# Kernel tuning notes

Measured on AMD Instinct MI355X. Metric: run time of the kernel, lower is better.

Reference implementation:

```python
import jax, jax.numpy as jnp
import numpy as np

N = 32768
E = 262144
OUT = 512
H = 8
DH = OUT // H


def setup_inputs() -> dict:
    key = jax.random.key(0)
    ks = jax.random.split(key, 12)
    s = 0.02
    return {
        "h": jax.random.normal(ks[0], (N, 512), dtype=jnp.float32),
        "row": jax.random.randint(ks[1], (E,), 0, N, dtype=jnp.int32),
        "col": jax.random.randint(ks[2], (E,), 0, N, dtype=jnp.int32),
        "W_in": jax.random.normal(ks[3], (512, OUT), dtype=jnp.float32) * s,
        "b_in": jnp.zeros((OUT,), dtype=jnp.float32),
        "W_q": jax.random.normal(ks[4], (OUT, OUT), dtype=jnp.float32) * s,
        "b_q": jnp.zeros((OUT,), dtype=jnp.float32),
        "W_k": jax.random.normal(ks[5], (OUT, OUT), dtype=jnp.float32) * s,
        "b_k": jnp.zeros((OUT,), dtype=jnp.float32),
        "W_v": jax.random.normal(ks[6], (OUT, OUT), dtype=jnp.float32) * s,
        "b_v": jnp.zeros((OUT,), dtype=jnp.float32),
    }


def reference(h, row, col, W_in, b_in, W_q, b_q, W_k, b_k, W_v, b_v):
    scaling = DH ** -0.5
    x = h @ W_in + b_in                                   # [N, OUT]
    q = ((x @ W_q + b_q) * scaling).reshape(N, H, DH)     # [N, H, DH]
    k = (x @ W_k + b_k).reshape(N, H, DH)
    v = (x @ W_v + b_v).reshape(N, H, DH)

    # bsddmm: per-edge, per-head attention logits only at adjacency nonzeros
    logits = jnp.einsum("ehd,ehd->eh", q[row], k[col])    # [E, H]

    # sparse row-wise softmax over each node's incident edges
    m = jax.ops.segment_max(logits, row, num_segments=N)  # [N, H]
    ex = jnp.exp(logits - m[row])                         # [E, H]
    denom = jax.ops.segment_sum(ex, row, num_segments=N)  # [N, H]
    attn = ex / denom[row]                                # [E, H]

    # bspmm: aggregate v over neighbors with sparse attention weights
    out = jax.ops.segment_sum(attn[:, :, None] * v[col], row, num_segments=N)  # [N, H, DH]
    return out
```

## Files before the change

kernel.cpp:

```cpp
#include <hip/hip_runtime.h>

#define NN 32768
#define EE 262144
#define DM 512
#define NQKV 1536
#define NHEAD 8
#define DHEAD 64

typedef unsigned short u16;
typedef unsigned int u32;
typedef __attribute__((ext_vector_type(8))) short bf16x8;
typedef __attribute__((ext_vector_type(4))) float f32x4;
typedef __attribute__((ext_vector_type(8))) u16 u16x8;
typedef __attribute__((ext_vector_type(4))) u32 u32x4;

__device__ __forceinline__ float bf2f(u16 u) {
  union { u32 i; float f; } x; x.i = ((u32)u) << 16; return x.f;
}
__device__ __forceinline__ float bflo(u32 p) {
  union { u32 i; float f; } x; x.i = p << 16; return x.f;
}
__device__ __forceinline__ float bfhi(u32 p) {
  union { u32 i; float f; } x; x.i = p & 0xFFFF0000u; return x.f;
}
__device__ __forceinline__ u16 f2bf(float f) {
  union { float f; u32 i; } x; x.f = f;
  u32 r = x.i + 0x7FFFu + ((x.i >> 16) & 1u);
  return (u16)(r >> 16);
}

__device__ __forceinline__ void load_lds16(const u16* g, u16* l) {
  __builtin_amdgcn_global_load_lds(
      (const __attribute__((address_space(1))) char*)(const void*)g,
      (__attribute__((address_space(3))) char*)(void*)l, 16, 0, 0);
}

__global__ void tcast_w(const float* __restrict__ Wq, const float* __restrict__ Wk,
                        const float* __restrict__ Wv, u16* __restrict__ At) {
  const int z = blockIdx.z;
  const float* W = (z == 0) ? Wq : (z == 1) ? Wk : Wv;
  const float scale = (z == 0) ? 0.125f : 1.0f;
  const int m0 = blockIdx.x * 64;
  const int j0 = blockIdx.y * 64;
  __shared__ float t[64][65];
  const int tx = threadIdx.x & 63, ty = threadIdx.x >> 6;
#pragma unroll
  for (int i = 0; i < 16; ++i) {
    const int r = ty * 16 + i;
    t[r][tx] = W[(size_t)(m0 + r) * 512 + (j0 + tx)];
  }
  __syncthreads();
#pragma unroll
  for (int i = 0; i < 16; ++i) {
    const int j = ty * 16 + i;
    At[(size_t)(z * 512 + j0 + j) * 512 + (m0 + tx)] = f2bf(t[tx][j] * scale);
  }
}

__global__ void cast_win(const float* __restrict__ Win, u16* __restrict__ Winb) {
  const int i = (blockIdx.x * 256 + threadIdx.x) * 8;
  float4 a = *(const float4*)&Win[i];
  float4 b = *(const float4*)&Win[i + 4];
  u16x8 o = { f2bf(a.x), f2bf(a.y), f2bf(a.z), f2bf(a.w),
              f2bf(b.x), f2bf(b.y), f2bf(b.z), f2bf(b.w) };
  *(u16x8*)&Winb[i] = o;
}

__global__ void make_bias(const float* __restrict__ bin,
                          const float* __restrict__ Wq, const float* __restrict__ bq,
                          const float* __restrict__ Wk, const float* __restrict__ bk,
                          const float* __restrict__ Wv, const float* __restrict__ bv,
                          float* __restrict__ bias) {
  const int j = blockIdx.x * 256 + threadIdx.x;
  if (j >= 1536) return;
  const float* Wsel; const float* bsel; int jj; float scale = 1.0f;
  if (j < 512)       { Wsel = Wq; bsel = bq; jj = j;        scale = 0.125f; }
  else if (j < 1024) { Wsel = Wk; bsel = bk; jj = j - 512;  }
  else               { Wsel = Wv; bsel = bv; jj = j - 1024; }
  float s = 0.f;
  for (int m = 0; m < 512; ++m) s = fmaf(bin[m], Wsel[m * 512 + jj], s);
  bias[j] = (s + bsel[jj]) * scale;
}

__global__ void cast_h(const float* __restrict__ h, u16* __restrict__ hb) {
  const int i = (blockIdx.x * 256 + threadIdx.x) * 8;
  float4 a = *(const float4*)&h[i];
  float4 b = *(const float4*)&h[i + 4];
  u16x8 o = { f2bf(a.x), f2bf(a.y), f2bf(a.z), f2bf(a.w),
              f2bf(b.x), f2bf(b.y), f2bf(b.z), f2bf(b.w) };
  *(u16x8*)&hb[i] = o;
}

__global__ void count_deg(const int* __restrict__ row, int* __restrict__ deg) {
  const int e = blockIdx.x * 256 + threadIdx.x;
  atomicAdd(&deg[row[e]], 1);
}

__global__ void scan_deg(const int* __restrict__ deg, int* __restrict__ row_ptr,
                         int* __restrict__ cursor) {
  __shared__ int sums[1024];
  const int t = threadIdx.x;
  const int base = t * 32;
  int loc[32];
  int s = 0;
#pragma unroll
  for (int i = 0; i < 32; ++i) { loc[i] = s; s += deg[base + i]; }
  sums[t] = s;
  __syncthreads();
  for (int off = 1; off < 1024; off <<= 1) {
    int v = (t >= off) ? sums[t - off] : 0;
    __syncthreads();
    sums[t] += v;
    __syncthreads();
  }
  const int excl = sums[t] - s;
#pragma unroll
  for (int i = 0; i < 32; ++i) {
    const int val = excl + loc[i];
    row_ptr[base + i] = val;
    cursor[base + i] = val;
  }
  if (t == 1023) row_ptr[NN] = sums[1023];
}

__global__ void fill_csr(const int* __restrict__ row, const int* __restrict__ col,
                         int* __restrict__ cursor, int* __restrict__ dst) {
  const int e = blockIdx.x * 256 + threadIdx.x;
  const int r = row[e];
  const int p = atomicAdd(&cursor[r], 1);
  dst[p] = col[e];
}

__global__ __launch_bounds__(256, 2) void gemm_wt(
    const u16* __restrict__ A,
    const u16* __restrict__ B,
    u16* __restrict__ C) {
  __shared__ u16 As[128 * 32];
  __shared__ u16 Bs[128 * 32];
  const int tid = threadIdx.x;
  const int lane = tid & 63;
  const int wave = tid >> 6;
  const int quad = lane >> 4;
  const int l16 = lane & 15;
  const int m0 = blockIdx.y * 128;
  const int n0 = blockIdx.x * 128;
  const int wm = (wave >> 1) * 64;
  const int wn = (wave & 1) * 64;

  const int c0 = tid, c1 = tid + 256;
  const int r0 = c0 >> 2, ko0 = (c0 & 3) * 8;
  const int r1 = c1 >> 2, ko1 = (c1 & 3) * 8;
  const u16* Ag0 = A + (size_t)(m0 + r0) * DM + ko0;
  const u16* Ag1 = A + (size_t)(m0 + r1) * DM + ko1;
  const u16* Bg0 = B + (size_t)(n0 + r0) * DM + ko0;
  const u16* Bg1 = B + (size_t)(n0 + r1) * DM + ko1;
  u16* Al0 = &As[c0 * 8]; u16* Al1 = &As[c1 * 8];
  u16* Bl0 = &Bs[c0 * 8]; u16* Bl1 = &Bs[c1 * 8];

  f32x4 acc[4][4];
#pragma unroll
  for (int i = 0; i < 4; ++i)
#pragma unroll
    for (int j = 0; j < 4; ++j) acc[i][j] = (f32x4){0.f, 0.f, 0.f, 0.f};

  for (int kt = 0; kt < DM; kt += 32) {
    load_lds16(Ag0 + kt, Al0);
    load_lds16(Bg0 + kt, Bl0);
    load_lds16(Ag1 + kt, Al1);
    load_lds16(Bg1 + kt, Bl1);
    __syncthreads();
    bf16x8 a[4], b[4];
#pragma unroll
    for (int i = 0; i < 4; ++i) {
      a[i] = *(const bf16x8*)&As[(wm + i * 16 + l16) * 32 + quad * 8];
      b[i] = *(const bf16x8*)&Bs[(wn + i * 16 + l16) * 32 + quad * 8];
    }
#pragma unroll
    for (int mi = 0; mi < 4; ++mi)
#pragma unroll
      for (int ni = 0; ni < 4; ++ni)
        acc[mi][ni] = __builtin_amdgcn_mfma_f32_16x16x32_bf16(a[mi], b[ni], acc[mi][ni], 0, 0, 0);
    __syncthreads();
  }

#pragma unroll
  for (int ni = 0; ni < 4; ++ni) {
    const int coln = n0 + wn + ni * 16 + l16;
#pragma unroll
    for (int mi = 0; mi < 4; ++mi) {
#pragma unroll
      for (int r = 0; r < 4; ++r) {
        const int rowm = m0 + wm + mi * 16 + quad * 4 + r;
        C[(size_t)rowm * 512 + coln] = f2bf(acc[mi][ni][r]);
      }
    }
  }
}

__global__ __launch_bounds__(256, 2) void gemm_qkv(
    const u16* __restrict__ A,
    const u16* __restrict__ B,
    const float* __restrict__ bias,
    u16* __restrict__ Cq,
    u16* __restrict__ Ckv) {
  __shared__ u16 As[128 * 32];
  __shared__ u16 Bs[128 * 32];
  const int tid = threadIdx.x;
  const int lane = tid & 63;
  const int wave = tid >> 6;
  const int quad = lane >> 4;
  const int l16 = lane & 15;
  const int m0 = blockIdx.y * 128;
  const int n0 = blockIdx.x * 128;
  const int wm = (wave >> 1) * 64;
  const int wn = (wave & 1) * 64;

  const int c0 = tid, c1 = tid + 256;
  const int r0 = c0 >> 2, ko0 = (c0 & 3) * 8;
  const int r1 = c1 >> 2, ko1 = (c1 & 3) * 8;
  const u16* Ag0 = A + (size_t)(m0 + r0) * DM + ko0;
  const u16* Ag1 = A + (size_t)(m0 + r1) * DM + ko1;
  const u16* Bg0 = B + (size_t)(n0 + r0) * DM + ko0;
  const u16* Bg1 = B + (size_t)(n0 + r1) * DM + ko1;
  u16* Al0 = &As[c0 * 8]; u16* Al1 = &As[c1 * 8];
  u16* Bl0 = &Bs[c0 * 8]; u16* Bl1 = &Bs[c1 * 8];

  f32x4 acc[4][4];
#pragma unroll
  for (int i = 0; i < 4; ++i)
#pragma unroll
    for (int j = 0; j < 4; ++j) acc[i][j] = (f32x4){0.f, 0.f, 0.f, 0.f};

  for (int kt = 0; kt < DM; kt += 32) {
    load_lds16(Ag0 + kt, Al0);
    load_lds16(Bg0 + kt, Bl0);
    load_lds16(Ag1 + kt, Al1);
    load_lds16(Bg1 + kt, Bl1);
    __syncthreads();
    bf16x8 a[4], b[4];
#pragma unroll
    for (int i = 0; i < 4; ++i) {
      a[i] = *(const bf16x8*)&As[(wm + i * 16 + l16) * 32 + quad * 8];
      b[i] = *(const bf16x8*)&Bs[(wn + i * 16 + l16) * 32 + quad * 8];
    }
#pragma unroll
    for (int mi = 0; mi < 4; ++mi)
#pragma unroll
      for (int ni = 0; ni < 4; ++ni)
        acc[mi][ni] = __builtin_amdgcn_mfma_f32_16x16x32_bf16(a[mi], b[ni], acc[mi][ni], 0, 0, 0);
    __syncthreads();
  }

#pragma unroll
  for (int ni = 0; ni < 4; ++ni) {
    const int coln = n0 + wn + ni * 16 + l16;
    const float bv = bias[coln];
    const int isq = coln < 512;
    const int sel = coln >= 1024;
    const int d = coln - 512 - (sel << 9);
#pragma unroll
    for (int mi = 0; mi < 4; ++mi) {
#pragma unroll
      for (int r = 0; r < 4; ++r) {
        const int rowm = m0 + wm + mi * 16 + quad * 4 + r;
        const u16 val = f2bf(acc[mi][ni][r] + bv);
        if (isq) Cq[(size_t)rowm * 512 + coln] = val;
        else     Ckv[(size_t)rowm * 1024 + d * 2 + sel] = val;
      }
    }
  }
}

__global__ __launch_bounds__(256) void attn_agg(
    const u16* __restrict__ q, const u32* __restrict__ kv,
    const int* __restrict__ row_ptr, const int* __restrict__ dst,
    float* __restrict__ out) {
  const int gt = blockIdx.x * 256 + threadIdx.x;
  const int node = gt >> 6;
  const int lane = gt & 63;
  const u16x8 qr = *(const u16x8*)&q[(size_t)node * 512 + lane * 8];
  float qf[8];
#pragma unroll
  for (int j = 0; j < 8; ++j) qf[j] = bf2f(qr[j]);

  const int beg = row_ptr[node];
  const int end = row_ptr[node + 1];
  float acc[8] = {0.f,0.f,0.f,0.f,0.f,0.f,0.f,0.f};
  float denom = 0.f;

  for (int e = beg; e < end; e += 4) {
    u32 p[4][8];
    int idx[4];
#pragma unroll
    for (int jj = 0; jj < 4; ++jj) {
      const int ee = min(e + jj, end - 1);
      idx[jj] = dst[ee];
    }
#pragma unroll
    for (int jj = 0; jj < 4; ++jj) {
      const u32* pp = kv + ((size_t)idx[jj] << 9) + lane * 8;
      *(u32x4*)&p[jj][0] = *(const u32x4*)pp;
      *(u32x4*)&p[jj][4] = *(const u32x4*)(pp + 4);
    }
#pragma unroll
    for (int jj = 0; jj < 4; ++jj) {
      float s = 0.f;
#pragma unroll
      for (int j = 0; j < 8; ++j) s = fmaf(qf[j], bflo(p[jj][j]), s);
      s += __shfl_xor(s, 1, 64);
      s += __shfl_xor(s, 2, 64);
      s += __shfl_xor(s, 4, 64);
      const float ex = (e + jj < end) ? __expf(s) : 0.f;
      denom += ex;
#pragma unroll
      for (int j = 0; j < 8; ++j) acc[j] = fmaf(ex, bfhi(p[jj][j]), acc[j]);
    }
  }

  const float inv = (end > beg) ? (1.0f / denom) : 0.f;
  float4 o0 = { acc[0] * inv, acc[1] * inv, acc[2] * inv, acc[3] * inv };
  float4 o1 = { acc[4] * inv, acc[5] * inv, acc[6] * inv, acc[7] * inv };
  float* op = &out[(size_t)node * 512 + lane * 8];
  *(float4*)op = o0;
  *(float4*)(op + 4) = o1;
}

extern "C" void kernel_launch(void* const* d_in, const int* in_sizes, int n_in,
                              void* d_out, int out_size, void* d_ws, size_t ws_size,
                              hipStream_t stream) {
  const float* h   = (const float*)d_in[0];
  const int*   row = (const int*)d_in[1];
  const int*   col = (const int*)d_in[2];
  const float* Win = (const float*)d_in[3];
  const float* bin = (const float*)d_in[4];
  const float* Wq  = (const float*)d_in[5];
  const float* bq  = (const float*)d_in[6];
  const float* Wk  = (const float*)d_in[7];
  const float* bk  = (const float*)d_in[8];
  const float* Wv  = (const float*)d_in[9];
  const float* bv  = (const float*)d_in[10];
  float* out = (float*)d_out;

  char* ws = (char*)d_ws;
  u16*   qbuf    = (u16*)(ws + 0);
  u16*   kvbuf   = (u16*)(ws + 33554432);
  u16*   hb      = (u16*)(ws + 100663296);
  u16*   Wt      = (u16*)(ws + 134217728);
  float* bias    = (float*)(ws + 135790592);
  int*   deg     = (int*)(ws + 135796736);
  int*   row_ptr = (int*)(ws + 135927808);
  int*   cursor  = (int*)(ws + 136058888);
  int*   dst     = (int*)(ws + 136189960);
  u16*   At      = (u16*)(ws + 0);
  u16*   Winb    = (u16*)(ws + 1572864);

  (void)hipMemsetAsync(deg, 0, NN * sizeof(int), stream);
  hipLaunchKernelGGL(tcast_w,   dim3(8, 8, 3), dim3(256), 0, stream, Wq, Wk, Wv, At);
  hipLaunchKernelGGL(cast_win,  dim3((512 * 512 / 8) / 256), dim3(256), 0, stream, Win, Winb);
  hipLaunchKernelGGL(make_bias, dim3(6), dim3(256), 0, stream, bin, Wq, bq, Wk, bk, Wv, bv, bias);
  hipLaunchKernelGGL(cast_h,    dim3((NN * DM / 8) / 256), dim3(256), 0, stream, h, hb);
  hipLaunchKernelGGL(count_deg, dim3(EE / 256), dim3(256), 0, stream, row, deg);
  hipLaunchKernelGGL(scan_deg,  dim3(1), dim3(1024), 0, stream, deg, row_ptr, cursor);
  hipLaunchKernelGGL(fill_csr,  dim3(EE / 256), dim3(256), 0, stream, row, col, cursor, dst);
  hipLaunchKernelGGL(gemm_wt,   dim3(512 / 128, 1536 / 128), dim3(256), 0, stream, At, Winb, Wt);
  hipLaunchKernelGGL(gemm_qkv,  dim3(NQKV / 128, NN / 128), dim3(256), 0, stream, hb, Wt, bias, qbuf, kvbuf);
  hipLaunchKernelGGL(attn_agg,  dim3((NN * 64) / 256), dim3(256), 0, stream,
                     qbuf, (const u32*)kvbuf, row_ptr, dst, out);
}
```

Measured before the change: 394.7 us.

## Swizzle GEMM LDS tiles and interleave K/V via weight row permutation

Applies an XOR swizzle to the LDS tile layout in both GEMMs so the MFMA fragment reads spread across banks instead of conflicting. It also permutes the fused weight and bias rows so K and V columns come out interleaved directly from the GEMM. That lets gemm_qkv write one contiguous [N,1536] output instead of scattered conditional stores, and attn_agg reads the interleaved KV from that unified buffer. The cost is a wider row stride (1536) for the gathered KV reads.

Result: faster. 379.1 us (-4.0%).

```diff
diff --git a/kernel.cpp b/kernel.cpp
--- a/kernel.cpp
+++ b/kernel.cpp
@@ -34,6 +34,11 @@
       (const __attribute__((address_space(1))) char*)(const void*)g,
       (__attribute__((address_space(3))) char*)(void*)l, 16, 0, 0);
 }
+
+__device__ __forceinline__ int swz(int r, int s) {
+  return s ^ (r & 3) ^ ((r >> 2) & 1);
+}
+
 
 __global__ void tcast_w(const float* __restrict__ Wq, const float* __restrict__ Wk,
                         const float* __restrict__ Wv, u16* __restrict__ At) {
@@ -52,8 +57,9 @@
   __syncthreads();
 #pragma unroll
   for (int i = 0; i < 16; ++i) {
-    const int j = ty * 16 + i;
-    At[(size_t)(z * 512 + j0 + j) * 512 + (m0 + tx)] = f2bf(t[tx][j] * scale);
+    const int j = j0 + ty * 16 + i;
+    const int pr = (z == 0) ? j : (512 + 2 * j + (z - 1));
+    At[(size_t)pr * 512 + (m0 + tx)] = f2bf(t[tx][ty * 16 + i] * scale);
   }
 }
 
@@ -73,13 +79,13 @@
                           float* __restrict__ bias) {
   const int j = blockIdx.x * 256 + threadIdx.x;
   if (j >= 1536) return;
-  const float* Wsel; const float* bsel; int jj; float scale = 1.0f;
-  if (j < 512)       { Wsel = Wq; bsel = bq; jj = j;        scale = 0.125f; }
-  else if (j < 1024) { Wsel = Wk; bsel = bk; jj = j - 512;  }
-  else               { Wsel = Wv; bsel = bv; jj = j - 1024; }
+  const float* Wsel; const float* bsel; int jj; float scale = 1.0f; int pos;
+  if (j < 512)       { Wsel = Wq; bsel = bq; jj = j;        scale = 0.125f; pos = j; }
+  else if (j < 1024) { Wsel = Wk; bsel = bk; jj = j - 512;  pos = 512 + 2 * jj; }
+  else               { Wsel = Wv; bsel = bv; jj = j - 1024; pos = 513 + 2 * jj; }
   float s = 0.f;
   for (int m = 0; m < 512; ++m) s = fmaf(bin[m], Wsel[m * 512 + jj], s);
-  bias[j] = (s + bsel[jj]) * scale;
+  bias[pos] = (s + bsel[jj]) * scale;
 }
 
 __global__ void cast_h(const float* __restrict__ h, u16* __restrict__ hb) {
@@ -148,8 +154,8 @@
   const int wn = (wave & 1) * 64;
 
   const int c0 = tid, c1 = tid + 256;
-  const int r0 = c0 >> 2, ko0 = (c0 & 3) * 8;
-  const int r1 = c1 >> 2, ko1 = (c1 & 3) * 8;
+  const int r0 = c0 >> 2, ko0 = swz(r0, c0 & 3) * 8;
+  const int r1 = c1 >> 2, ko1 = swz(r1, c1 & 3) * 8;
   const u16* Ag0 = A + (size_t)(m0 + r0) * DM + ko0;
   const u16* Ag1 = A + (size_t)(m0 + r1) * DM + ko1;
   const u16* Bg0 = B + (size_t)(n0 + r0) * DM + ko0;
@@ -172,8 +178,10 @@
     bf16x8 a[4], b[4];
 #pragma unroll
     for (int i = 0; i < 4; ++i) {
-      a[i] = *(const bf16x8*)&As[(wm + i * 16 + l16) * 32 + quad * 8];
-      b[i] = *(const bf16x8*)&Bs[(wn + i * 16 + l16) * 32 + quad * 8];
+      const int ra = wm + i * 16 + l16;
+      const int rb = wn + i * 16 + l16;
+      a[i] = *(const bf16x8*)&As[ra * 32 + swz(ra, quad) * 8];
+      b[i] = *(const bf16x8*)&Bs[rb * 32 + swz(rb, quad) * 8];
     }
 #pragma unroll
     for (int mi = 0; mi < 4; ++mi)
@@ -201,8 +209,7 @@
     const u16* __restrict__ A,
     const u16* __restrict__ B,
     const float* __restrict__ bias,
-    u16* __restrict__ Cq,
-    u16* __restrict__ Ckv) {
+    u16* __restrict__ C) {
   __shared__ u16 As[128 * 32];
   __shared__ u16 Bs[128 * 32];
   const int tid = threadIdx.x;
@@ -216,8 +223,8 @@
   const int wn = (wave & 1) * 64;
 
   const int c0 = tid, c1 = tid + 256;
-  const int r0 = c0 >> 2, ko0 = (c0 & 3) * 8;
-  const int r1 = c1 >> 2, ko1 = (c1 & 3) * 8;
+  const int r0 = c0 >> 2, ko0 = swz(r0, c0 & 3) * 8;
+  const int r1 = c1 >> 2, ko1 = swz(r1, c1 & 3) * 8;
   const u16* Ag0 = A + (size_t)(m0 + r0) * DM + ko0;
   const u16* Ag1 = A + (size_t)(m0 + r1) * DM + ko1;
   const u16* Bg0 = B + (size_t)(n0 + r0) * DM + ko0;
@@ -240,8 +247,10 @@
     bf16x8 a[4], b[4];
 #pragma unroll
     for (int i = 0; i < 4; ++i) {
-      a[i] = *(const bf16x8*)&As[(wm + i * 16 + l16) * 32 + quad * 8];
-      b[i] = *(const bf16x8*)&Bs[(wn + i * 16 + l16) * 32 + quad * 8];
+      const int ra = wm + i * 16 + l16;
+      const int rb = wn + i * 16 + l16;
+      a[i] = *(const bf16x8*)&As[ra * 32 + swz(ra, quad) * 8];
+      b[i] = *(const bf16x8*)&Bs[rb * 32 + swz(rb, quad) * 8];
     }
 #pragma unroll
     for (int mi = 0; mi < 4; ++mi)
@@ -255,30 +264,25 @@
   for (int ni = 0; ni < 4; ++ni) {
     const int coln = n0 + wn + ni * 16 + l16;
     const float bv = bias[coln];
-    const int isq = coln < 512;
-    const int sel = coln >= 1024;
-    const int d = coln - 512 - (sel << 9);
 #pragma unroll
     for (int mi = 0; mi < 4; ++mi) {
 #pragma unroll
       for (int r = 0; r < 4; ++r) {
         const int rowm = m0 + wm + mi * 16 + quad * 4 + r;
-        const u16 val = f2bf(acc[mi][ni][r] + bv);
-        if (isq) Cq[(size_t)rowm * 512 + coln] = val;
-        else     Ckv[(size_t)rowm * 1024 + d * 2 + sel] = val;
+        C[(size_t)rowm * NQKV + coln] = f2bf(acc[mi][ni][r] + bv);
       }
     }
   }
 }
 
 __global__ __launch_bounds__(256) void attn_agg(
-    const u16* __restrict__ q, const u32* __restrict__ kv,
+    const u16* __restrict__ qkv16, const u32* __restrict__ qkv32,
     const int* __restrict__ row_ptr, const int* __restrict__ dst,
     float* __restrict__ out) {
   const int gt = blockIdx.x * 256 + threadIdx.x;
   const int node = gt >> 6;
   const int lane = gt & 63;
-  const u16x8 qr = *(const u16x8*)&q[(size_t)node * 512 + lane * 8];
+  const u16x8 qr = *(const u16x8*)&qkv16[(size_t)node * NQKV + lane * 8];
   float qf[8];
 #pragma unroll
   for (int j = 0; j < 8; ++j) qf[j] = bf2f(qr[j]);
@@ -298,7 +302,7 @@
     }
 #pragma unroll
     for (int jj = 0; jj < 4; ++jj) {
-      const u32* pp = kv + ((size_t)idx[jj] << 9) + lane * 8;
+      const u32* pp = qkv32 + (size_t)idx[jj] * 768 + 256 + lane * 8;
       *(u32x4*)&p[jj][0] = *(const u32x4*)pp;
       *(u32x4*)&p[jj][4] = *(const u32x4*)(pp + 4);
     }
@@ -342,8 +346,7 @@
   float* out = (float*)d_out;
 
   char* ws = (char*)d_ws;
-  u16*   qbuf    = (u16*)(ws + 0);
-  u16*   kvbuf   = (u16*)(ws + 33554432);
+  u16*   qkv     = (u16*)(ws + 0);
   u16*   hb      = (u16*)(ws + 100663296);
   u16*   Wt      = (u16*)(ws + 134217728);
   float* bias    = (float*)(ws + 135790592);
@@ -363,7 +366,7 @@
   hipLaunchKernelGGL(scan_deg,  dim3(1), dim3(1024), 0, stream, deg, row_ptr, cursor);
   hipLaunchKernelGGL(fill_csr,  dim3(EE / 256), dim3(256), 0, stream, row, col, cursor, dst);
   hipLaunchKernelGGL(gemm_wt,   dim3(512 / 128, 1536 / 128), dim3(256), 0, stream, At, Winb, Wt);
-  hipLaunchKernelGGL(gemm_qkv,  dim3(NQKV / 128, NN / 128), dim3(256), 0, stream, hb, Wt, bias, qbuf, kvbuf);
+  hipLaunchKernelGGL(gemm_qkv,  dim3(NQKV / 128, NN / 128), dim3(256), 0, stream, hb, Wt, bias, qkv);
   hipLaunchKernelGGL(attn_agg,  dim3((NN * 64) / 256), dim3(256), 0, stream,
-                     qbuf, (const u32*)kvbuf, row_ptr, dst, out);
-}
+                     qkv, (const u32*)qkv, row_ptr, dst, out);
+}
```
